# Kernel optimization log

Hardware: AMD Instinct MI355X
Metric: run time of the kernel (lower is better)

Reference implementation:

```python
import jax, jax.numpy as jnp
import numpy as np

B, S, N = 16, 512, 321          # batch, input length, n_variates (dec_in)
D, DF, LAYERS = 512, 2048, 2    # d_model, d_ff, e_layers
M, K, P = 3, 3, 96              # wavelet levels, kernel_size, pred_len
ALPHA = 0.3


def _dwconv(x, h, dilation):
    # x: [B, C, L], h: [C, K] depthwise dilated conv (cross-correlation, like torch)
    return jax.lax.conv_general_dilated(
        x, h[:, None, :], window_strides=(1,), padding='VALID',
        rhs_dilation=(dilation,), dimension_numbers=('NCH', 'OIH', 'NCH'),
        feature_group_count=x.shape[1])


def _swt_dec(x, h0, h1):
    # stationary wavelet decomposition; x: [B, N, D] -> [B, N, M+1, D]
    approx, coeffs, dil = x, [], 1
    for _ in range(M):
        pad_total = dil * (K - 1)
        pad_r = (K * dil) // 2
        xp = jnp.pad(approx, ((0, 0), (0, 0), (pad_total - pad_r, pad_r)), mode='wrap')
        coeffs.append(_dwconv(xp, h1, dil))
        approx = _dwconv(xp, h0, dil)
        dil *= 2
    coeffs.append(approx)
    return jnp.stack(coeffs[::-1], axis=-2)


def _swt_rec(c, g0, g1):
    # inverse SWT; c: [B, N, M+1, D] -> [B, N, D]
    approx = c[:, :, 0, :]
    dil = 2 ** (M - 1)
    for i in range(M):
        det = c[:, :, 1 + i, :]
        pad_total = dil * (K - 1)
        pad_l = (dil * K) // 2
        pads = ((0, 0), (0, 0), (pad_l, pad_total - pad_l))
        approx = (_dwconv(jnp.pad(approx, pads, mode='wrap'), g0, dil)
                  + _dwconv(jnp.pad(det, pads, mode='wrap'), g1, dil)) / 2
        dil //= 2
    return approx


def _geom_attention(q, k, v):
    # q,k,v: [B, L=D, H=M+1, E=N]
    scale = 1.0 / jnp.sqrt(jnp.float32(q.shape[-1]))
    dot = jnp.einsum('blhe,bshe->bhls', q, k)
    qn2 = jnp.sum(q * q, -1).transpose(0, 2, 1)  # [B,H,L]
    kn2 = jnp.sum(k * k, -1).transpose(0, 2, 1)  # [B,H,S]
    wedge = jnp.sqrt(jax.nn.relu(qn2[:, :, :, None] * kn2[:, :, None, :] - dot * dot) + 1e-8)
    scores = ((1.0 - ALPHA) * dot + ALPHA * wedge) * scale
    A = jax.nn.softmax(scores, axis=-1)
    return jnp.einsum('bhls,bshd->blhd', A, v)


def _layernorm(x, g, b, eps=1e-5):
    mu = x.mean(-1, keepdims=True)
    var = jnp.mean((x - mu) ** 2, -1, keepdims=True)
    return (x - mu) / jnp.sqrt(var + eps) * g + b


def _forward(x_enc, emb_W, emb_b, h0, h1, g0, g1, Wq, bq, Wk, bk, Wv, bv, Wo, bo,
             W1, b1, W2, b2, ln1_g, ln1_b, ln2_g, ln2_b, lnf_g, lnf_b, proj_W, proj_b):
    # RevIN-style normalize (means detached as in torch code)
    means = jax.lax.stop_gradient(x_enc.mean(1, keepdims=True))
    stdev = jnp.sqrt(x_enc.var(1, keepdims=True) + 1e-5)
    x = (x_enc - means) / stdev
    # inverted embedding: each variate's full series -> d_model token
    h = jnp.einsum('bsn,ds->bnd', x, emb_W) + emb_b  # [B,N,D]
    for l in range(LAYERS):
        coeffs = _swt_dec(h, h0[l], h1[l])  # [B,N,M+1,D]
        q = (jnp.einsum('bnmd,ed->bnme', coeffs, Wq[l]) + bq[l]).transpose(0, 3, 2, 1)
        kk = (jnp.einsum('bnmd,ed->bnme', coeffs, Wk[l]) + bk[l]).transpose(0, 3, 2, 1)
        vv = (jnp.einsum('bnmd,ed->bnme', coeffs, Wv[l]) + bv[l]).transpose(0, 3, 2, 1)
        out = _geom_attention(q, kk, vv).transpose(0, 3, 2, 1)  # [B,N,M+1,D]
        out = _swt_rec(out, g0[l], g1[l])                        # [B,N,D]
        out = jnp.einsum('bnd,ed->bne', out, Wo[l]) + bo[l]
        x1 = _layernorm(h + out, ln1_g[l], ln1_b[l])
        y = jax.nn.gelu(jnp.einsum('bnd,fd->bnf', x1, W1[l]) + b1[l], approximate=False)
        y = jnp.einsum('bnf,df->bnd', y, W2[l]) + b2[l]
        h = _layernorm(x1 + y, ln2_g[l], ln2_b[l])
    h = _layernorm(h, lnf_g, lnf_b)
    dec = (jnp.einsum('bnd,pd->bnp', h, proj_W) + proj_b).transpose(0, 2, 1)  # [B,P,N]
    dec = dec * stdev[:, 0, :][:, None, :] + means[:, 0, :][:, None, :]
    return dec, means, stdev


def setup_inputs():
    key = jax.random.key(0)
    ks = jax.random.split(key, 24)
    def filt(k):
        f = jax.random.normal(k, (LAYERS, N, K), jnp.float32)
        return f / jnp.linalg.norm(f, axis=-1, keepdims=True)
    w = lambda k, shape: jax.random.normal(k, shape, jnp.float32) * 0.02
    z = lambda shape: jnp.zeros(shape, jnp.float32)
    o = lambda shape: jnp.ones(shape, jnp.float32)
    return {
        'x_enc': jax.random.normal(ks[0], (B, S, N), jnp.float32),
        'emb_W': w(ks[1], (D, S)), 'emb_b': z((D,)),
        'h0': filt(ks[2]), 'h1': filt(ks[3]), 'g0': filt(ks[4]), 'g1': filt(ks[5]),
        'Wq': w(ks[6], (LAYERS, D, D)), 'bq': z((LAYERS, D)),
        'Wk': w(ks[7], (LAYERS, D, D)), 'bk': z((LAYERS, D)),
        'Wv': w(ks[8], (LAYERS, D, D)), 'bv': z((LAYERS, D)),
        'Wo': w(ks[9], (LAYERS, D, D)), 'bo': z((LAYERS, D)),
        'W1': w(ks[10], (LAYERS, DF, D)), 'b1': z((LAYERS, DF)),
        'W2': w(ks[11], (LAYERS, D, DF)), 'b2': z((LAYERS, D)),
        'ln1_g': o((LAYERS, D)), 'ln1_b': z((LAYERS, D)),
        'ln2_g': o((LAYERS, D)), 'ln2_b': z((LAYERS, D)),
        'lnf_g': o((D,)), 'lnf_b': z((D,)),
        'proj_W': w(ks[12], (P, D)), 'proj_b': z((P,)),
    }


def reference(x_enc, emb_W, emb_b, h0, h1, g0, g1, Wq, bq, Wk, bk, Wv, bv, Wo, bo,
              W1, b1, W2, b2, ln1_g, ln1_b, ln2_g, ln2_b, lnf_g, lnf_b, proj_W, proj_b):
    return _forward(x_enc, emb_W, emb_b, h0, h1, g0, g1, Wq, bq, Wk, bk, Wv, bv, Wo, bo,
                    W1, b1, W2, b2, ln1_g, ln1_b, ln2_g, ln2_b, lnf_g, lnf_b, proj_W, proj_b)
```

## Files before the change

kernel.cpp:

```cpp
#include <hip/hip_runtime.h>
#include <hip/hip_bf16.h>
#include <math.h>
#include <stdint.h>

#define Bn 16
#define Sn 512
#define Nn 321
#define Dn 512
#define DFn 2048
#define Pn 96
#define KP 352

typedef __bf16 bf16x8 __attribute__((ext_vector_type(8)));
typedef float f32x4 __attribute__((ext_vector_type(4)));
typedef __hip_bfloat16 bf16;

static __device__ __forceinline__ float gelu_exact(float x) {
    return 0.5f * x * (1.0f + erff(x * 0.7071067811865476f));
}

static __device__ __forceinline__ void gld16(const void* g, void* l) {
    __builtin_amdgcn_global_load_lds(
        (const __attribute__((address_space(1))) void*)(uintptr_t)g,
        (__attribute__((address_space(3))) void*)(uintptr_t)l, 16, 0, 0);
}

struct CvtPack {
    const float* src[14];
    bf16* dst[14];
    int cnt[14];
};
__global__ void cvt_all_kernel(CvtPack p) {
    int seg = blockIdx.y;
    int n = p.cnt[seg];
    const float* s = p.src[seg];
    bf16* d = p.dst[seg];
    int i = (blockIdx.x * 256 + threadIdx.x) * 4;
    if (i + 3 < n) {
        float4 v = *reinterpret_cast<const float4*>(s + i);
        d[i] = __float2bfloat16(v.x);
        d[i + 1] = __float2bfloat16(v.y);
        d[i + 2] = __float2bfloat16(v.z);
        d[i + 3] = __float2bfloat16(v.w);
    }
}

__global__ void bias_pack_kernel(const float* __restrict__ bq, const float* __restrict__ bk,
                                 float* __restrict__ bqk) {
    int idx = blockIdx.x * 256 + threadIdx.x;
    if (idx >= 2048) return;
    int l = idx >> 10, j = idx & 1023;
    bqk[idx] = (j < 512) ? bq[l * 512 + j] : bk[l * 512 + j - 512];
}

__global__ void stats_kernel(const float* __restrict__ x, float* __restrict__ means,
                             float* __restrict__ stdev) {
    int b = blockIdx.y;
    int n = blockIdx.x * 256 + threadIdx.x;
    if (n >= Nn) return;
    const float* p = x + (size_t)b * Sn * Nn + n;
    float s = 0.f, s2 = 0.f;
    for (int ss = 0; ss < Sn; ++ss) { float v = p[(size_t)ss * Nn]; s += v; s2 += v * v; }
    float mu = s * (1.0f / Sn);
    float var = s2 * (1.0f / Sn) - mu * mu;
    means[b * Nn + n] = mu;
    stdev[b * Nn + n] = sqrtf(var + 1e-5f);
}

__global__ void transpose_norm_kernel(const float* __restrict__ x,
                                      const float* __restrict__ means,
                                      const float* __restrict__ stdev,
                                      bf16* __restrict__ xT) {
    __shared__ float tile[32][33];
    int b = blockIdx.z;
    int s0 = blockIdx.x * 32, n0 = blockIdx.y * 32;
    int tx = threadIdx.x, ty = threadIdx.y;
#pragma unroll
    for (int u = 0; u < 4; ++u) {
        int srow = ty + u * 8;
        int n = n0 + tx;
        tile[srow][tx] = (n < Nn) ? x[((size_t)b * Sn + (s0 + srow)) * Nn + n] : 0.f;
    }
    __syncthreads();
#pragma unroll
    for (int u = 0; u < 4; ++u) {
        int n = n0 + ty + u * 8;
        int s = s0 + tx;
        if (n < Nn) {
            float mu = means[b * Nn + n], sd = stdev[b * Nn + n];
            xT[((size_t)b * Nn + n) * Sn + s] = __float2bfloat16((tile[tx][ty + u * 8] - mu) / sd);
        }
    }
}

template <int OUT, int EPI>
__global__ __launch_bounds__(256) void mm_kernel(
    const bf16* __restrict__ A, const bf16* __restrict__ Bm,
    const float* __restrict__ bias, void* __restrict__ C,
    int Mdim, int Ndim, int Kdim, int lda, int ldb, int ldc,
    long sAi, long sAo, long sBi, long sBo, long sCi, long sCo, int innerB) {
    int z = blockIdx.z;
    int zi = z % innerB, zo = z / innerB;
    const bf16* Ab = A + (size_t)zi * sAi + (size_t)zo * sAo;
    const bf16* Bb = Bm + (size_t)zi * sBi + (size_t)zo * sBo;
    __shared__ __align__(16) bf16 As[128 * 32];
    __shared__ __align__(16) bf16 Bs[128 * 32];
    int t = threadIdx.x;
    int wave = t >> 6, lane = t & 63;
    int wr = wave >> 1, wc = wave & 1;
    int q = lane >> 4, l16 = lane & 15;
    int i0 = blockIdx.y * 128, j0 = blockIdx.x * 128;

    int srow0 = t >> 2;
    int scol = (t & 3) * 8;
    f32x4 acc[4][4] = {};

    for (int k0 = 0; k0 < Kdim; k0 += 32) {
#pragma unroll
        for (int u = 0; u < 2; ++u) {
            int row = u * 64 + srow0;
            int gcol = scol ^ (((row >> 1) & 3) << 3);
            int gi = i0 + row; if (gi >= Mdim) gi = Mdim - 1;
            gld16(Ab + (size_t)gi * lda + k0 + gcol, &As[u * 2048 + wave * 512]);
            int gj = j0 + row; if (gj >= Ndim) gj = Ndim - 1;
            gld16(Bb + (size_t)gj * ldb + k0 + gcol, &Bs[u * 2048 + wave * 512]);
        }
        __syncthreads();
        bf16x8 af[4], bfr[4];
#pragma unroll
        for (int mi = 0; mi < 4; ++mi) {
            int r = wr * 64 + mi * 16 + l16;
            int cl = (q * 8) ^ (((r >> 1) & 3) << 3);
            af[mi] = *reinterpret_cast<const bf16x8*>(&As[r * 32 + cl]);
        }
#pragma unroll
        for (int ni = 0; ni < 4; ++ni) {
            int r = wc * 64 + ni * 16 + l16;
            int cl = (q * 8) ^ (((r >> 1) & 3) << 3);
            bfr[ni] = *reinterpret_cast<const bf16x8*>(&Bs[r * 32 + cl]);
        }
#pragma unroll
        for (int mi = 0; mi < 4; ++mi)
#pragma unroll
            for (int ni = 0; ni < 4; ++ni)
                acc[mi][ni] = __builtin_amdgcn_mfma_f32_16x16x32_bf16(af[mi], bfr[ni], acc[mi][ni], 0, 0, 0);
        __syncthreads();
    }
    size_t cbase = (size_t)zi * sCi + (size_t)zo * sCo;
#pragma unroll
    for (int mi = 0; mi < 4; ++mi) {
#pragma unroll
        for (int r = 0; r < 4; ++r) {
            int gi = i0 + wr * 64 + mi * 16 + q * 4 + r;
            if (gi >= Mdim) continue;
#pragma unroll
            for (int ni = 0; ni < 4; ++ni) {
                int gj = j0 + wc * 64 + ni * 16 + l16;
                if (gj >= Ndim) continue;
                float v = acc[mi][ni][r];
                if (bias) v += bias[gj];
                if (EPI == 1) v = gelu_exact(v);
                size_t cidx = cbase + (size_t)gi * ldc + gj;
                if (OUT == 0) ((float*)C)[cidx] = v;
                else ((bf16*)C)[cidx] = __float2bfloat16(v);
            }
        }
    }
}

__global__ __launch_bounds__(128) void swt_dec_kernel(
    const float* __restrict__ h, const float* __restrict__ h0f,
    const float* __restrict__ h1f, bf16* __restrict__ coeffs) {
    __shared__ float a[2][512];
    int b = blockIdx.y, n = blockIdx.x, t = threadIdx.x;
    const float* hrow = h + ((size_t)b * Nn + n) * Dn;
#pragma unroll
    for (int u = 0; u < 4; ++u) a[0][t + u * 128] = hrow[t + u * 128];
    float f0[3], f1[3];
#pragma unroll
    for (int k = 0; k < 3; ++k) { f0[k] = h0f[n * 3 + k]; f1[k] = h1f[n * 3 + k]; }
    __syncthreads();
    bf16* cb = coeffs + ((size_t)b * Nn + n) * 4 * Dn;
    int cur = 0;
    for (int lev = 0; lev < 3; ++lev) {
        int dil = 1 << lev;
        int pl = 2 * dil - (3 * dil) / 2;
#pragma unroll
        for (int u = 0; u < 4; ++u) {
            int d = t + u * 128;
            float dv = 0.f, av = 0.f;
#pragma unroll
            for (int k = 0; k < 3; ++k) {
                int idx = (d + k * dil - pl) & 511;
                float xv = a[cur][idx];
                dv += f1[k] * xv;
                av += f0[k] * xv;
            }
            cb[(size_t)(3 - lev) * Dn + d] = __float2bfloat16(dv);
            a[cur ^ 1][d] = av;
        }
        __syncthreads();
        cur ^= 1;
    }
#pragma unroll
    for (int u = 0; u < 4; ++u) cb[t + u * 128] = __float2bfloat16(a[cur][t + u * 128]);
}

__global__ __launch_bounds__(128) void swt_rec_kernel(
    const bf16* __restrict__ attn, const float* __restrict__ g0f,
    const float* __restrict__ g1f, bf16* __restrict__ rec) {
    __shared__ float a[2][512];
    __shared__ float det[512];
    int b = blockIdx.y, n = blockIdx.x, t = threadIdx.x;
    const bf16* base = attn + ((size_t)(b * 4) * Nn + n) * Dn;
#pragma unroll
    for (int u = 0; u < 4; ++u) a[0][t + u * 128] = __bfloat162float(base[t + u * 128]);
    float w0[3], w1[3];
#pragma unroll
    for (int k = 0; k < 3; ++k) { w0[k] = g0f[n * 3 + k]; w1[k] = g1f[n * 3 + k]; }
    int cur = 0;
    for (int i = 0; i < 3; ++i) {
        int dil = 4 >> i;
        int pl = (3 * dil) / 2;
        const bf16* drow = base + (size_t)(1 + i) * Nn * Dn;
#pragma unroll
        for (int u = 0; u < 4; ++u) det[t + u * 128] = __bfloat162float(drow[t + u * 128]);
        __syncthreads();
#pragma unroll
        for (int u = 0; u < 4; ++u) {
            int d = t + u * 128;
            float s = 0.f;
#pragma unroll
            for (int k = 0; k < 3; ++k) {
                int idx = (d + k * dil - pl) & 511;
                s += w0[k] * a[cur][idx] + w1[k] * det[idx];
            }
            a[cur ^ 1][d] = s * 0.5f;
        }
        __syncthreads();
        cur ^= 1;
    }
    bf16* out = rec + ((size_t)b * Nn + n) * Dn;
#pragma unroll
    for (int u = 0; u < 4; ++u) out[t + u * 128] = __float2bfloat16(a[cur][t + u * 128]);
}

__global__ void tconv2_kernel(const bf16* __restrict__ QK, bf16* __restrict__ QtKt) {
    __shared__ bf16 tile[32][33];
    int zz = blockIdx.z;
    int qk = zz >> 6, bm = zz & 63;
    int b = bm >> 2, m = bm & 3;
    int e0 = blockIdx.x * 32, n0 = blockIdx.y * 32;
    int tx = threadIdx.x, ty = threadIdx.y;
    const bf16* ib = QK + (size_t)b * Nn * 4096 + (size_t)m * 1024 + (size_t)qk * 512;
    bf16* ob = QtKt + (size_t)qk * 64 * 512 * KP + (size_t)bm * 512 * KP;
#pragma unroll
    for (int u = 0; u < 4; ++u) {
        int n = n0 + ty + u * 8;
        bf16 v = __float2bfloat16(0.f);
        if (n < Nn) v = ib[(size_t)n * 4096 + e0 + tx];
        tile[ty + u * 8][tx] = v;
    }
    __syncthreads();
#pragma unroll
    for (int u = 0; u < 4; ++u) {
        int e = e0 + ty + u * 8;
        int n = n0 + tx;
        if (n < KP) ob[(size_t)e * KP + n] = tile[tx][ty + u * 8];
    }
}

__global__ __launch_bounds__(256) void colsq2_kernel(const bf16* __restrict__ QK,
                                                     float* __restrict__ outv) {
    int y = blockIdx.y;
    int qk = y >> 6, bm = y & 63;
    int b = bm >> 2, m = bm & 3;
    int e0 = blockIdx.x * 64;
    int tx = threadIdx.x & 63, ty = threadIdx.x >> 6;
    const bf16* base = QK + ((size_t)b * Nn * 4 + m) * 1024 + (size_t)qk * 512;
    float s = 0.f;
    for (int n = ty; n < Nn; n += 4) {
        float v = __bfloat162float(base[(size_t)n * 4096 + e0 + tx]);
        s += v * v;
    }
    __shared__ float red[4][64];
    red[ty][tx] = s;
    __syncthreads();
    if (ty == 0)
        outv[(size_t)qk * 32768 + (size_t)bm * 512 + e0 + tx] =
            red[0][tx] + red[1][tx] + red[2][tx] + red[3][tx];
}

__global__ __launch_bounds__(256) void wedge_softmax_kernel(
    bf16* __restrict__ Smat, const float* __restrict__ qn2, const float* __restrict__ kn2) {
    int bm = blockIdx.y, l = blockIdx.x, t = threadIdx.x;
    bf16* row = Smat + ((size_t)bm * 512 + l) * 512;
    const float* kn = kn2 + (size_t)bm * 512;
    float q2 = qn2[(size_t)bm * 512 + l];
    const float scale = rsqrtf(321.0f);
    float v[2];
    float mx = -1e30f;
#pragma unroll
    for (int u = 0; u < 2; ++u) {
        int s = t + u * 256;
        float d = __bfloat162float(row[s]);
        float w = sqrtf(fmaxf(q2 * kn[s] - d * d, 0.f) + 1e-8f);
        float sc = (0.7f * d + 0.3f * w) * scale;
        v[u] = sc;
        mx = fmaxf(mx, sc);
    }
    __shared__ float red[256];
    red[t] = mx;
    __syncthreads();
    for (int o = 128; o > 0; o >>= 1) {
        if (t < o) red[t] = fmaxf(red[t], red[t + o]);
        __syncthreads();
    }
    mx = red[0];
    __syncthreads();
    float sum = 0.f;
#pragma unroll
    for (int u = 0; u < 2; ++u) {
        v[u] = expf(v[u] - mx);
        sum += v[u];
    }
    red[t] = sum;
    __syncthreads();
    for (int o = 128; o > 0; o >>= 1) {
        if (t < o) red[t] += red[t + o];
        __syncthreads();
    }
    float inv = 1.0f / red[0];
#pragma unroll
    for (int u = 0; u < 2; ++u) row[t + u * 256] = __float2bfloat16(v[u] * inv);
}

__global__ __launch_bounds__(128) void ln_kernel(
    const float* __restrict__ A, const float* __restrict__ R, const float* __restrict__ R2,
    const float* __restrict__ g, const float* __restrict__ bb,
    float* __restrict__ outf, bf16* __restrict__ outb) {
    size_t r = blockIdx.x;
    int t = threadIdx.x;
    const float* ra = A + r * Dn;
    float x[4];
    float s = 0.f, s2 = 0.f;
#pragma unroll
    for (int u = 0; u < 4; ++u) {
        int d = t + u * 128;
        float v = ra[d];
        if (R) v += R[r * Dn + d];
        if (R2) v += R2[r * Dn + d];
        x[u] = v;
        s += v;
        s2 += v * v;
    }
    __shared__ float rs[128], rs2[128];
    rs[t] = s;
    rs2[t] = s2;
    __syncthreads();
    for (int o = 64; o > 0; o >>= 1) {
        if (t < o) { rs[t] += rs[t + o]; rs2[t] += rs2[t + o]; }
        __syncthreads();
    }
    float mean = rs[0] * (1.0f / Dn);
    float var = rs2[0] * (1.0f / Dn) - mean * mean;
    float inv = rsqrtf(var + 1e-5f);
#pragma unroll
    for (int u = 0; u < 4; ++u) {
        int d = t + u * 128;
        float v = (x[u] - mean) * inv * g[d] + bb[d];
        if (outf) outf[r * Dn + d] = v;
        if (outb) outb[r * Dn + d] = __float2bfloat16(v);
    }
}

__global__ void out_scale_kernel(const float* __restrict__ ptmp,
                                 const float* __restrict__ means,
                                 const float* __restrict__ stdev, float* __restrict__ dec) {
    int idx = blockIdx.x * 256 + threadIdx.x;
    if (idx >= Bn * Pn * Nn) return;
    int n = idx % Nn;
    int bp = idx / Nn;
    int p = bp % Pn;
    int b = bp / Pn;
    const size_t PS = (size_t)Bn * Nn * Pn;
    size_t base = ((size_t)b * Nn + n) * Pn + p;
    float v = ptmp[base] + ptmp[base + PS] + ptmp[base + 2 * PS] + ptmp[base + 3 * PS];
    dec[idx] = v * stdev[b * Nn + n] + means[b * Nn + n];
}

extern "C" void kernel_launch(void* const* d_in, const int* in_sizes, int n_in,
                              void* d_out, int out_size, void* d_ws, size_t ws_size,
                              hipStream_t stream) {
    const float* x_enc = (const float*)d_in[0];
    const float* emb_W = (const float*)d_in[1];
    const float* emb_b = (const float*)d_in[2];
    const float* h0 = (const float*)d_in[3];
    const float* h1 = (const float*)d_in[4];
    const float* g0 = (const float*)d_in[5];
    const float* g1 = (const float*)d_in[6];
    const float* Wq = (const float*)d_in[7];
    const float* bq = (const float*)d_in[8];
    const float* Wk = (const float*)d_in[9];
    const float* bk = (const float*)d_in[10];
    const float* Wv = (const float*)d_in[11];
    const float* bv = (const float*)d_in[12];
    const float* Wo = (const float*)d_in[13];
    const float* bo = (const float*)d_in[14];
    const float* W1 = (const float*)d_in[15];
    const float* b1 = (const float*)d_in[16];
    const float* W2 = (const float*)d_in[17];
    const float* b2 = (const float*)d_in[18];
    const float* ln1_g = (const float*)d_in[19];
    const float* ln1_b = (const float*)d_in[20];
    const float* ln2_g = (const float*)d_in[21];
    const float* ln2_b = (const float*)d_in[22];
    const float* lnf_g = (const float*)d_in[23];
    const float* lnf_b = (const float*)d_in[24];
    const float* proj_W = (const float*)d_in[25];
    const float* proj_b = (const float*)d_in[26];

    float* dec = (float*)d_out;
    float* means = dec + (size_t)Bn * Pn * Nn;
    float* stdev = means + (size_t)Bn * Nn;

    char* p = (char*)d_ws;
    auto alloc = [&](size_t bytes) { char* r = p; p += (bytes + 255) & ~(size_t)255; return r; };
    const size_t RD = (size_t)Bn * Nn * Dn;
    const size_t RQ4 = RD * 4;

    bf16* embWb = (bf16*)alloc(262144 * 2);
    bf16* Wqkb = (bf16*)alloc(2 * 524288 * 2);
    bf16* Wvb = (bf16*)alloc(2 * 262144 * 2);
    bf16* Wob = (bf16*)alloc(2 * 262144 * 2);
    bf16* W1b = (bf16*)alloc(2 * 1048576 * 2);
    bf16* W2b = (bf16*)alloc(2 * 1048576 * 2);
    bf16* projWb = (bf16*)alloc(49152 * 2);
    float* bqk = (float*)alloc(2048 * 4);

    float* hbuf = (float*)alloc(RD * 4);
    char* regC = alloc(RQ4 * 2);
    char* regQ = alloc(RQ4 * 2);
    char* regK = alloc(RQ4 * 2);
    char* regV = alloc(RQ4 * 2);
    char* regT = alloc((size_t)2 * 64 * 512 * KP * 2);
    float* qn2 = (float*)alloc((size_t)2 * 64 * 512 * 4);
    float* kn2 = qn2 + 32768;

    bf16* coeffs_b = (bf16*)regC;
    bf16* attn_b = (bf16*)regC;
    bf16* QK0b = (bf16*)regQ;
    bf16* Smat = (bf16*)regQ;
    bf16* recb = (bf16*)regQ;
    bf16* x1b = (bf16*)(regQ + RD * 2);
    float* ptmp = (float*)regQ;
    bf16* V0b = (bf16*)regV;
    bf16* yb = (bf16*)regV;
    bf16* QtKt = (bf16*)regT;
    bf16* Qt = QtKt;
    bf16* Kt = QtKt + (size_t)64 * 512 * KP;
    bf16* xT_b = (bf16*)regT;
    float* x1 = (float*)regT;
    float* tmp = (float*)(regT + RD * 4);
    bf16* hfb = (bf16*)(regT + RD * 12);

    const int R = Bn * Nn;
    const int RQr = R * 4;
    const long sbm = (long)4 * Nn * 512;
    const long sS = (long)512 * 512;
    const long sTq = (long)512 * KP;
    const long sTb = 4 * sTq;

    CvtPack cp;
    int ci = 0;
    auto addcvt = [&](const float* s, bf16* d, int n) { cp.src[ci] = s; cp.dst[ci] = d; cp.cnt[ci] = n; ++ci; };
    addcvt(emb_W, embWb, 262144);
    for (int l = 0; l < 2; ++l) {
        addcvt(Wq + (size_t)l * 262144, Wqkb + (size_t)l * 524288, 262144);
        addcvt(Wk + (size_t)l * 262144, Wqkb + (size_t)l * 524288 + 262144, 262144);
        addcvt(Wv + (size_t)l * 262144, Wvb + (size_t)l * 262144, 262144);
        addcvt(Wo + (size_t)l * 262144, Wob + (size_t)l * 262144, 262144);
        addcvt(W1 + (size_t)l * 1048576, W1b + (size_t)l * 1048576, 1048576);
        addcvt(W2 + (size_t)l * 1048576, W2b + (size_t)l * 1048576, 1048576);
    }
    addcvt(proj_W, projWb, 49152);
    cvt_all_kernel<<<dim3(1048576 / 4 / 256, 14), 256, 0, stream>>>(cp);
    bias_pack_kernel<<<8, 256, 0, stream>>>(bq, bk, bqk);

    stats_kernel<<<dim3((Nn + 255) / 256, Bn), 256, 0, stream>>>(x_enc, means, stdev);
    transpose_norm_kernel<<<dim3(Sn / 32, (Nn + 31) / 32, Bn), dim3(32, 8), 0, stream>>>(
        x_enc, means, stdev, xT_b);

    mm_kernel<0, 0><<<dim3(4, (R + 127) / 128, 1), 256, 0, stream>>>(
        xT_b, embWb, emb_b, hbuf, R, Dn, Sn, Sn, Sn, Dn, 0, 0, 0, 0, 0, 0, 1);

    for (int l = 0; l < 2; ++l) {
        const float* h0l = h0 + (size_t)l * Nn * 3;
        const float* h1l = h1 + (size_t)l * Nn * 3;
        const float* g0l = g0 + (size_t)l * Nn * 3;
        const float* g1l = g1 + (size_t)l * Nn * 3;

        swt_dec_kernel<<<dim3(Nn, Bn), 128, 0, stream>>>(hbuf, h0l, h1l, coeffs_b);

        mm_kernel<1, 0><<<dim3(8, (RQr + 127) / 128, 1), 256, 0, stream>>>(
            coeffs_b, Wqkb + (size_t)l * 524288, bqk + (size_t)l * 1024, QK0b,
            RQr, 1024, Dn, Dn, Dn, 1024, 0, 0, 0, 0, 0, 0, 1);
        mm_kernel<1, 0><<<dim3(4, (RQr + 127) / 128, 1), 256, 0, stream>>>(
            coeffs_b, Wvb + (size_t)l * 262144, bv + (size_t)l * Dn, V0b,
            RQr, Dn, Dn, Dn, Dn, Dn, 0, 0, 0, 0, 0, 0, 1);

        colsq2_kernel<<<dim3(8, 128), 256, 0, stream>>>(QK0b, qn2);
        tconv2_kernel<<<dim3(16, 11, 128), dim3(32, 8), 0, stream>>>(QK0b, QtKt);

        mm_kernel<1, 0><<<dim3(4, 4, 64), 256, 0, stream>>>(
            Qt, Kt, nullptr, Smat, 512, 512, KP, KP, KP, 512,
            sTq, sTb, sTq, sTb, sS, 4 * sS, 4);

        wedge_softmax_kernel<<<dim3(512, 64), 256, 0, stream>>>(Smat, qn2, kn2);

        mm_kernel<1, 0><<<dim3(4, (Nn + 127) / 128, 64), 256, 0, stream>>>(
            V0b, Smat, nullptr, attn_b, Nn, 512, 512, 2048, 512, 512,
            512, sbm, sS, 4 * sS, (long)Nn * 512, (long)4 * Nn * 512, 4);

        swt_rec_kernel<<<dim3(Nn, Bn), 128, 0, stream>>>(attn_b, g0l, g1l, recb);

        mm_kernel<0, 0><<<dim3(4, (R + 127) / 128, 2), 256, 0, stream>>>(
            recb, Wob + (size_t)l * 262144, bo + (size_t)l * Dn, tmp,
            R, Dn, 256, Dn, Dn, Dn, 256, 0, 256, 0, (long)RD, 0, 2);
        ln_kernel<<<R, 128, 0, stream>>>(hbuf, tmp, tmp + RD, ln1_g + (size_t)l * Dn,
                                         ln1_b + (size_t)l * Dn, x1, x1b);

        mm_kernel<1, 1><<<dim3(16, (R + 127) / 128, 1), 256, 0, stream>>>(
            x1b, W1b + (size_t)l * 1048576, b1 + (size_t)l * DFn, yb,
            R, DFn, Dn, Dn, Dn, DFn, 0, 0, 0, 0, 0, 0, 1);
        mm_kernel<0, 0><<<dim3(4, (R + 127) / 128, 2), 256, 0, stream>>>(
            yb, W2b + (size_t)l * 1048576, b2 + (size_t)l * Dn, tmp,
            R, Dn, 1024, DFn, DFn, Dn, 1024, 0, 1024, 0, (long)RD, 0, 2);
        ln_kernel<<<R, 128, 0, stream>>>(x1, tmp, tmp + RD, ln2_g + (size_t)l * Dn,
                                         ln2_b + (size_t)l * Dn, hbuf, nullptr);
    }

    ln_kernel<<<R, 128, 0, stream>>>(hbuf, nullptr, nullptr, lnf_g, lnf_b, nullptr, hfb);
    mm_kernel<0, 0><<<dim3(1, (R + 127) / 128, 4), 256, 0, stream>>>(
        hfb, projWb, proj_b, ptmp, R, Pn, 128, Dn, Dn, Pn,
        128, 0, 128, 0, (long)R * Pn, 0, 4);
    out_scale_kernel<<<(Bn * Pn * Nn + 255) / 256, 256, 0, stream>>>(ptmp, means, stdev, dec);
}
```

Before: 1.003 ms.

## Double-buffer GEMM LDS tiles and group block order for L2 reuse

The bf16 MFMA GEMM kernel now uses two LDS buffers for the A and B tiles. It issues the global-to-LDS loads for the next K slice right after the barrier, so they overlap the MFMAs on the current slice, and it drops one of the two barriers per iteration. Thread blocks are also remapped so that groups of 8 row-tiles walk the column tiles together, which is meant to improve L2 reuse of the shared operand. LDS use per block doubles, which may lower occupancy.

```diff
diff --git a/kernel.cpp b/kernel.cpp
--- a/kernel.cpp
+++ b/kernel.cpp
@@ -103,48 +103,69 @@
     int zi = z % innerB, zo = z / innerB;
     const bf16* Ab = A + (size_t)zi * sAi + (size_t)zo * sAo;
     const bf16* Bb = Bm + (size_t)zi * sBi + (size_t)zo * sBo;
-    __shared__ __align__(16) bf16 As[128 * 32];
-    __shared__ __align__(16) bf16 Bs[128 * 32];
+
+    int gx = gridDim.x, gy = gridDim.y;
+    int lin = blockIdx.y * gx + blockIdx.x;
+    int prefix = (gy & ~7) * gx;
+    int bx, by;
+    if (lin < prefix) {
+        bx = (lin >> 3) % gx;
+        by = (lin / (8 * gx)) * 8 + (lin & 7);
+    } else {
+        int r = lin - prefix;
+        bx = r % gx;
+        by = (gy & ~7) + r / gx;
+    }
+
+    __shared__ __align__(16) bf16 As[2][128 * 32];
+    __shared__ __align__(16) bf16 Bs[2][128 * 32];
     int t = threadIdx.x;
     int wave = t >> 6, lane = t & 63;
     int wr = wave >> 1, wc = wave & 1;
     int q = lane >> 4, l16 = lane & 15;
-    int i0 = blockIdx.y * 128, j0 = blockIdx.x * 128;
+    int i0 = by * 128, j0 = bx * 128;
 
     int srow0 = t >> 2;
     int scol = (t & 3) * 8;
     f32x4 acc[4][4] = {};
 
-    for (int k0 = 0; k0 < Kdim; k0 += 32) {
+    int nIter = Kdim >> 5;
+
+    auto stage = [&](int k0, int buf) {
 #pragma unroll
         for (int u = 0; u < 2; ++u) {
             int row = u * 64 + srow0;
             int gcol = scol ^ (((row >> 1) & 3) << 3);
             int gi = i0 + row; if (gi >= Mdim) gi = Mdim - 1;
-            gld16(Ab + (size_t)gi * lda + k0 + gcol, &As[u * 2048 + wave * 512]);
+            gld16(Ab + (size_t)gi * lda + k0 + gcol, &As[buf][u * 2048 + wave * 512]);
             int gj = j0 + row; if (gj >= Ndim) gj = Ndim - 1;
-            gld16(Bb + (size_t)gj * ldb + k0 + gcol, &Bs[u * 2048 + wave * 512]);
-        }
-        __syncthreads();
+            gld16(Bb + (size_t)gj * ldb + k0 + gcol, &Bs[buf][u * 2048 + wave * 512]);
+        }
+    };
+
+    stage(0, 0);
+    for (int it = 0; it < nIter; ++it) {
+        __syncthreads();
+        if (it + 1 < nIter) stage((it + 1) << 5, (it + 1) & 1);
+        int buf = it & 1;
         bf16x8 af[4], bfr[4];
 #pragma unroll
         for (int mi = 0; mi < 4; ++mi) {
             int r = wr * 64 + mi * 16 + l16;
             int cl = (q * 8) ^ (((r >> 1) & 3) << 3);
-            af[mi] = *reinterpret_cast<const bf16x8*>(&As[r * 32 + cl]);
+            af[mi] = *reinterpret_cast<const bf16x8*>(&As[buf][r * 32 + cl]);
         }
 #pragma unroll
         for (int ni = 0; ni < 4; ++ni) {
             int r = wc * 64 + ni * 16 + l16;
             int cl = (q * 8) ^ (((r >> 1) & 3) << 3);
-            bfr[ni] = *reinterpret_cast<const bf16x8*>(&Bs[r * 32 + cl]);
+            bfr[ni] = *reinterpret_cast<const bf16x8*>(&Bs[buf][r * 32 + cl]);
         }
 #pragma unroll
         for (int mi = 0; mi < 4; ++mi)
 #pragma unroll
             for (int ni = 0; ni < 4; ++ni)
                 acc[mi][ni] = __builtin_amdgcn_mfma_f32_16x16x32_bf16(af[mi], bfr[ni], acc[mi][ni], 0, 0, 0);
-        __syncthreads();
     }
     size_t cbase = (size_t)zi * sCi + (size_t)zo * sCo;
 #pragma unroll
```

New measurement: 914.8 us. -8.8%, faster.
